# Optimization experiments

Hardware: AMD Instinct MI355X
Metric: run time of the kernel (lower is better)

The kernel has to match this reference:

```python
import jax, jax.numpy as jnp
import numpy as np

NS = 16384   # N*S support examples
NQ = 16384   # N*Q query examples
D = 64       # embedding dim
N_CLASSES = 64


def setup_inputs() -> dict:
    key = jax.random.key(0)
    k1, k2, k3 = jax.random.split(key, 3)
    support_embeddings = jax.random.normal(k1, (NS, D), dtype=jnp.float32)
    query_embeddings = jax.random.normal(k2, (NQ, D), dtype=jnp.float32)
    labels = jax.random.randint(k3, (NS,), 0, N_CLASSES)
    support_labels_onehot = jax.nn.one_hot(labels, N_CLASSES, dtype=jnp.float32)
    return {
        "support_embeddings": support_embeddings,
        "query_embeddings": query_embeddings,
        "support_labels_onehot": support_labels_onehot,
    }


def reference(support_embeddings, query_embeddings, support_labels_onehot):
    # Pairwise L2 distance via ||q||^2 + ||s||^2 - 2 q.s (same math as
    # tf.norm(q[:,None,:] - s[None,:,:], axis=2) without the [NQ,NS,D] blowup).
    sq_s = jnp.sum(support_embeddings * support_embeddings, axis=-1)  # [NS]
    sq_q = jnp.sum(query_embeddings * query_embeddings, axis=-1)      # [NQ]
    cross = jnp.einsum('qd,sd->qs', query_embeddings, support_embeddings)  # [NQ,NS]
    d2 = sq_q[:, None] + sq_s[None, :] - 2.0 * cross
    distance = jnp.sqrt(jnp.maximum(d2, 0.0))
    # top_k(-distance, k=1) == first argmin along support axis
    indices = jnp.argmin(distance, axis=1)                 # [NQ]
    labels_x = jnp.argmax(support_labels_onehot, axis=1)   # [NS]
    labels_pred = labels_x[indices]                        # [NQ] gather
    num_classes = support_labels_onehot.shape[1]
    labels_prob = jax.nn.one_hot(labels_pred, num_classes, dtype=support_labels_onehot.dtype)
    return labels_prob
```

## Files before the change

### kernel.cpp

```cpp
#include <hip/hip_runtime.h>


#define NTOT   16384
#define DIM    64
#define EPS_COEF 0.004f
#define EPS_ABS  0.05f
#define CINIT_COEF (-0.499f)
#define FLT_BIG 3.4e38f

typedef __attribute__((ext_vector_type(8))) short short8;
typedef __attribute__((ext_vector_type(4))) float float4v;

__device__ __forceinline__ ushort f16_bits(float x) {
  union { _Float16 f; ushort u; } c;
  c.f = (_Float16)x;
  return c.u;
}

__device__ __forceinline__ void pin8(short8& v) {
  asm volatile("" : "+v"(v));
}

__global__ __launch_bounds__(256) void k_prep(
    const float* __restrict__ S, const float* __restrict__ Q,
    ushort* __restrict__ Sh, ushort* __restrict__ Qh,
    float* __restrict__ sqS, float* __restrict__ sqQ,
    float* __restrict__ S_T) {
  __shared__ float tile[64][65];
  const int tid = threadIdx.x;
  const bool isS = blockIdx.x < 256;
  const int rbase = (blockIdx.x & 255) * 64;
  const float* __restrict__ src = isS ? S : Q;
  ushort* __restrict__ dh = isS ? Sh : Qh;

  const int tx = tid & 63;
  const int ty = tid >> 6;
#pragma unroll
  for (int i = 0; i < 16; ++i) {
    const int r = i * 4 + ty;
    tile[r][tx] = src[(size_t)(rbase + r) * DIM + tx];
  }
  __syncthreads();

  if (isS) {
#pragma unroll
    for (int i = 0; i < 16; ++i) {
      const int d = i * 4 + ty;
      S_T[(size_t)d * NTOT + rbase + tx] = tile[tx][d];
    }
  }

  const int panel = tid >> 6;
  const int half = (tid >> 5) & 1;
  const int slot0 = (tid & 31) * 2;
#pragma unroll
  for (int ss = 0; ss < 2; ++ss) {
    const int s = slot0 + ss;
    const int m = s & 15;
    const int q8 = s >> 4;
    const int row = panel * 16 + m;
    const int kb = half * 32 + q8 * 8;
    short8 hv;
#pragma unroll
    for (int j = 0; j < 8; ++j) hv[j] = (short)f16_bits(tile[row][kb + j]);
    const size_t goff =
        (size_t)((rbase >> 4) + panel) * 1024 + (size_t)half * 512 + (size_t)s * 8;
    *(short8*)&dh[goff] = hv;
  }

  if (tid < 64) {
    float acc = 0.0f;
#pragma unroll
    for (int d = 0; d < DIM; ++d) {
      const float v = tile[tid][d];
      acc = fmaf(v, v, acc);
    }
    (isS ? sqS : sqQ)[rbase + tid] = acc;
  }
}


#define MFMA16F(A, B, C) __builtin_amdgcn_mfma_f32_16x16x32_f16(A, B, C, 0, 0, 0)

#define STEP_COMPUTE(H0, H1, SQ)                                           \
  do {                                                                     \
    float4v cinit;                                                         \
    cinit[0] = CINIT_COEF * SQ.x;                                          \
    cinit[1] = CINIT_COEF * SQ.y;                                          \
    cinit[2] = CINIT_COEF * SQ.z;                                          \
    cinit[3] = CINIT_COEF * SQ.w;                                          \
    _Pragma("unroll")                                                      \
    for (int t = 0; t < 4; ++t) {                                          \
      float4v a = MFMA16F(H0, qh[t][0], cinit);                            \
      a = MFMA16F(H1, qh[t][1], a);                                        \
      bmr[t] = fmaxf(bmr[t], fmaxf(fmaxf(a[0], a[1]), fmaxf(a[2], a[3]))); \
    }                                                                      \
  } while (0)

template <int BST>
__global__ __launch_bounds__(256, 3) void k_phaseA(
    const ushort* __restrict__ Sh, const ushort* __restrict__ Qh,
    const float* __restrict__ sqS, float* __restrict__ bmin) {
  constexpr int NSB = NTOT / (16 * BST);
  const int tid = threadIdx.x;
  const int l = tid & 63;
  const int w = tid >> 6;
  const int lm = l & 15;
  const int lq = l >> 4;
  const int split = blockIdx.x;
  const int qbase = blockIdx.y * 64;
  const int sbase = split * 2048 + w * 512;

  short8 qh[4][2];
#pragma unroll
  for (int t = 0; t < 4; ++t) {
    const size_t pb = (size_t)((qbase >> 4) + t) * 1024 + (size_t)l * 8;
    qh[t][0] = *(const short8*)&Qh[pb];
    qh[t][1] = *(const short8*)&Qh[pb + 512];
  }
#pragma unroll
  for (int t = 0; t < 4; ++t) {
    pin8(qh[t][0]);
    pin8(qh[t][1]);
  }

  const ushort* pSh = Sh + (size_t)(sbase >> 4) * 1024 + (size_t)l * 8;
  const float* psq = sqS + sbase + lq * 4;

  short8 h0a = *(const short8*)(pSh);
  short8 h1a = *(const short8*)(pSh + 512);
  float4 sqa = *(const float4*)(psq);
  short8 h0b = *(const short8*)(pSh + 1024);
  short8 h1b = *(const short8*)(pSh + 1024 + 512);
  float4 sqb = *(const float4*)(psq + 16);

  float bmr[4] = {-FLT_BIG, -FLT_BIG, -FLT_BIG, -FLT_BIG};

  for (int st = 0; st < 32; st += 2) {
    STEP_COMPUTE(h0a, h1a, sqa);
    if (st + 2 < 32) {
      const int off = (st + 2) * 1024;
      h0a = *(const short8*)(pSh + off);
      h1a = *(const short8*)(pSh + off + 512);
      sqa = *(const float4*)(psq + (st + 2) * 16);
    }
    STEP_COMPUTE(h0b, h1b, sqb);
    if (st + 3 < 32) {
      const int off = (st + 3) * 1024;
      h0b = *(const short8*)(pSh + off);
      h1b = *(const short8*)(pSh + off + 512);
      sqb = *(const float4*)(psq + (st + 3) * 16);
    }
    if (((st + 1) & (BST - 1)) == (BST - 1)) {
      const int gb = split * (128 / BST) + w * (32 / BST) + ((st + 1) / BST);
#pragma unroll
      for (int t = 0; t < 4; ++t) {
        float v = bmr[t];
        v = fmaxf(v, __shfl_xor(v, 16, 64));
        v = fmaxf(v, __shfl_xor(v, 32, 64));
        if (lq == 0) bmin[(size_t)(qbase + t * 16 + lm) * NSB + gb] = -2.0f * v;
        bmr[t] = -FLT_BIG;
      }
    }
  }
}

template <int SBLK>
__global__ __launch_bounds__(256) void k_phaseB(
    const float* __restrict__ S_T,
    const float* __restrict__ Q,
    const float* __restrict__ sqS, const float* __restrict__ sqQ,
    const float* __restrict__ bmin,
    const float* __restrict__ onehot, float* __restrict__ out) {
  constexpr int NSB = NTOT / SBLK;
  constexpr int NB64 = NSB / 64;
  constexpr int SPL = SBLK / 64;

  __shared__ float sQrow[4][64];
  const int lane = threadIdx.x & 63;
  const int w = threadIdx.x >> 6;
  const int q = blockIdx.x * 4 + w;

  if (lane < 16)
    *(float4*)&sQrow[w][lane * 4] = *(const float4*)&Q[(size_t)q * DIM + lane * 4];
  __syncthreads();

  const float eps = EPS_COEF * sqQ[q] + EPS_ABS;

  float bv[NB64];
#pragma unroll
  for (int j = 0; j < NB64; ++j) bv[j] = bmin[(size_t)q * NSB + j * 64 + lane];
  float m = bv[0];
#pragma unroll
  for (int j = 1; j < NB64; ++j) m = fminf(m, bv[j]);
#pragma unroll
  for (int d = 1; d < 64; d <<= 1) m = fminf(m, __shfl_xor(m, d, 64));
  const float thr = m + eps;

  float bk = FLT_BIG;
  int bi = 0;
#pragma unroll
  for (int j = 0; j < NB64; ++j) {
    unsigned long long msk = __ballot(bv[j] <= thr);
    while (msk) {
      const int b = j * 64 + (__ffsll((long long)msk) - 1);
      msk &= msk - 1;
      const int s0 = b * SBLK + lane * SPL;
      if (SPL == 2) {
        float a0 = 0.f, a1 = 0.f;
#pragma unroll
        for (int c = 0; c < 16; ++c) {
          const float4 qv = *(const float4*)&sQrow[w][c * 4];
          const float2 x0 = *(const float2*)&S_T[(size_t)(c * 4 + 0) * NTOT + s0];
          const float2 x1 = *(const float2*)&S_T[(size_t)(c * 4 + 1) * NTOT + s0];
          const float2 x2 = *(const float2*)&S_T[(size_t)(c * 4 + 2) * NTOT + s0];
          const float2 x3 = *(const float2*)&S_T[(size_t)(c * 4 + 3) * NTOT + s0];
          a0 = fmaf(qv.x, x0.x, a0); a1 = fmaf(qv.x, x0.y, a1);
          a0 = fmaf(qv.y, x1.x, a0); a1 = fmaf(qv.y, x1.y, a1);
          a0 = fmaf(qv.z, x2.x, a0); a1 = fmaf(qv.z, x2.y, a1);
          a0 = fmaf(qv.w, x3.x, a0); a1 = fmaf(qv.w, x3.y, a1);
        }
        const float2 sq2 = *(const float2*)&sqS[s0];
        const float k0 = fmaf(-2.f, a0, sq2.x);
        const float k1 = fmaf(-2.f, a1, sq2.y);
        bool u;
        u = k0 < bk; bk = u ? k0 : bk; bi = u ? s0 : bi;
        u = k1 < bk; bk = u ? k1 : bk; bi = u ? (s0 + 1) : bi;
      } else {
        float a0 = 0.f, a1 = 0.f, a2 = 0.f, a3 = 0.f;
#pragma unroll
        for (int c = 0; c < 16; ++c) {
          const float4 qv = *(const float4*)&sQrow[w][c * 4];
          const float4 s0v = *(const float4*)&S_T[(size_t)(c * 4 + 0) * NTOT + s0];
          const float4 s1v = *(const float4*)&S_T[(size_t)(c * 4 + 1) * NTOT + s0];
          const float4 s2v = *(const float4*)&S_T[(size_t)(c * 4 + 2) * NTOT + s0];
          const float4 s3v = *(const float4*)&S_T[(size_t)(c * 4 + 3) * NTOT + s0];
          a0 = fmaf(qv.x, s0v.x, a0); a1 = fmaf(qv.x, s0v.y, a1);
          a2 = fmaf(qv.x, s0v.z, a2); a3 = fmaf(qv.x, s0v.w, a3);
          a0 = fmaf(qv.y, s1v.x, a0); a1 = fmaf(qv.y, s1v.y, a1);
          a2 = fmaf(qv.y, s1v.z, a2); a3 = fmaf(qv.y, s1v.w, a3);
          a0 = fmaf(qv.z, s2v.x, a0); a1 = fmaf(qv.z, s2v.y, a1);
          a2 = fmaf(qv.z, s2v.z, a2); a3 = fmaf(qv.z, s2v.w, a3);
          a0 = fmaf(qv.w, s3v.x, a0); a1 = fmaf(qv.w, s3v.y, a1);
          a2 = fmaf(qv.w, s3v.z, a2); a3 = fmaf(qv.w, s3v.w, a3);
        }
        const float4 sq4 = *(const float4*)&sqS[s0];
        const float k0 = fmaf(-2.f, a0, sq4.x);
        const float k1 = fmaf(-2.f, a1, sq4.y);
        const float k2 = fmaf(-2.f, a2, sq4.z);
        const float k3 = fmaf(-2.f, a3, sq4.w);
        bool u;
        u = k0 < bk; bk = u ? k0 : bk; bi = u ? s0 : bi;
        u = k1 < bk; bk = u ? k1 : bk; bi = u ? (s0 + 1) : bi;
        u = k2 < bk; bk = u ? k2 : bk; bi = u ? (s0 + 2) : bi;
        u = k3 < bk; bk = u ? k3 : bk; bi = u ? (s0 + 3) : bi;
      }
    }
  }
#pragma unroll
  for (int d = 1; d < 64; d <<= 1) {
    const float ok = __shfl_xor(bk, d, 64);
    const int oi = __shfl_xor(bi, d, 64);
    const bool u = (ok < bk) || (ok == bk && oi < bi);
    bk = u ? ok : bk;
    bi = u ? oi : bi;
  }
  const float ov = onehot[(size_t)bi * 64 + lane];
  const unsigned long long lmask = __ballot(ov > 0.5f);
  const int label = __ffsll((long long)lmask) - 1;
  out[(size_t)q * 64 + lane] = (lane == label) ? 1.0f : 0.0f;
}

extern "C" void kernel_launch(void* const* d_in, const int* in_sizes, int n_in,
                              void* d_out, int out_size, void* d_ws, size_t ws_size,
                              hipStream_t stream) {
  const float* S = (const float*)d_in[0];
  const float* Q = (const float*)d_in[1];
  const float* OH = (const float*)d_in[2];
  float* out = (float*)d_out;

  char* ws = (char*)d_ws;
  ushort* Sh = (ushort*)ws;
  ushort* Qh = (ushort*)(ws + (2u << 20));
  float* S_T = (float*)(ws + (4u << 20));
  float* sqS = (float*)(ws + (8u << 20));
  float* sqQ = (float*)(ws + (8u << 20) + (64u << 10));
  float* bmin = (float*)(ws + (8u << 20) + (128u << 10));

  k_prep<<<dim3(512), 256, 0, stream>>>(S, Q, Sh, Qh, sqS, sqQ, S_T);

  if (ws_size >= (17u << 20)) {
    k_phaseA<8><<<dim3(8, NTOT / 64), 256, 0, stream>>>(Sh, Qh, sqS, bmin);
    k_phaseB<128><<<dim3(NTOT / 4), 256, 0, stream>>>(S_T, Q, sqS, sqQ,
                                                      bmin, OH, out);
  } else {
    k_phaseA<16><<<dim3(8, NTOT / 64), 256, 0, stream>>>(Sh, Qh, sqS, bmin);
    k_phaseB<256><<<dim3(NTOT / 4), 256, 0, stream>>>(S_T, Q, sqS, sqQ,
                                                      bmin, OH, out);
  }
  (void)in_sizes; (void)n_in; (void)out_size; (void)ws_size;
}
```

Baseline: 153.3 us.

## Fuse prep and both phases into one cooperative persistent kernel with grid syncs

Merges the three kernel launches into a single cooperative kernel. It loops over virtual blocks for each stage and uses grid-wide syncs between prep, phase A and phase B. The aim is to remove launch overhead and the inter-kernel drain/fill gaps. In exchange, each block runs with fixed occupancy across all phases (launch bounds of 4 blocks per CU instead of 3 for phase A), pays for grid.sync, and issues host-side attribute and occupancy queries on every call.

```diff
diff --git a/kernel.cpp b/kernel.cpp
--- a/kernel.cpp
+++ b/kernel.cpp
@@ -1,4 +1,7 @@
 #include <hip/hip_runtime.h>
+#include <hip/hip_cooperative_groups.h>
+
+namespace cg = cooperative_groups;
 
 
 #define NTOT   16384
@@ -21,15 +24,15 @@
   asm volatile("" : "+v"(v));
 }
 
-__global__ __launch_bounds__(256) void k_prep(
-    const float* __restrict__ S, const float* __restrict__ Q,
+
+__device__ __forceinline__ void prep_body(
+    int vb, const float* __restrict__ S, const float* __restrict__ Q,
     ushort* __restrict__ Sh, ushort* __restrict__ Qh,
     float* __restrict__ sqS, float* __restrict__ sqQ,
-    float* __restrict__ S_T) {
-  __shared__ float tile[64][65];
+    float* __restrict__ S_T, float (*tile)[65]) {
   const int tid = threadIdx.x;
-  const bool isS = blockIdx.x < 256;
-  const int rbase = (blockIdx.x & 255) * 64;
+  const bool isS = vb < 256;
+  const int rbase = (vb & 255) * 64;
   const float* __restrict__ src = isS ? S : Q;
   ushort* __restrict__ dh = isS ? Sh : Qh;
 
@@ -77,8 +80,8 @@
     }
     (isS ? sqS : sqQ)[rbase + tid] = acc;
   }
-}
-
+  __syncthreads();
+}
 
 #define MFMA16F(A, B, C) __builtin_amdgcn_mfma_f32_16x16x32_f16(A, B, C, 0, 0, 0)
 
@@ -98,17 +101,16 @@
   } while (0)
 
 template <int BST>
-__global__ __launch_bounds__(256, 3) void k_phaseA(
-    const ushort* __restrict__ Sh, const ushort* __restrict__ Qh,
-    const float* __restrict__ sqS, float* __restrict__ bmin) {
+__device__ __forceinline__ void phaseA_body(
+    int split, int qbase, const ushort* __restrict__ Sh,
+    const ushort* __restrict__ Qh, const float* __restrict__ sqS,
+    float* __restrict__ bmin) {
   constexpr int NSB = NTOT / (16 * BST);
   const int tid = threadIdx.x;
   const int l = tid & 63;
   const int w = tid >> 6;
   const int lm = l & 15;
   const int lq = l >> 4;
-  const int split = blockIdx.x;
-  const int qbase = blockIdx.y * 64;
   const int sbase = split * 2048 + w * 512;
 
   short8 qh[4][2];
@@ -166,20 +168,18 @@
 }
 
 template <int SBLK>
-__global__ __launch_bounds__(256) void k_phaseB(
-    const float* __restrict__ S_T,
-    const float* __restrict__ Q,
+__device__ __forceinline__ void phaseB_body(
+    int u, const float* __restrict__ S_T, const float* __restrict__ Q,
     const float* __restrict__ sqS, const float* __restrict__ sqQ,
-    const float* __restrict__ bmin,
-    const float* __restrict__ onehot, float* __restrict__ out) {
+    const float* __restrict__ bmin, const float* __restrict__ onehot,
+    float* __restrict__ out, float (*sQrow)[64]) {
   constexpr int NSB = NTOT / SBLK;
   constexpr int NB64 = NSB / 64;
   constexpr int SPL = SBLK / 64;
 
-  __shared__ float sQrow[4][64];
   const int lane = threadIdx.x & 63;
   const int w = threadIdx.x >> 6;
-  const int q = blockIdx.x * 4 + w;
+  const int q = u * 4 + w;
 
   if (lane < 16)
     *(float4*)&sQrow[w][lane * 4] = *(const float4*)&Q[(size_t)q * DIM + lane * 4];
@@ -223,9 +223,9 @@
         const float2 sq2 = *(const float2*)&sqS[s0];
         const float k0 = fmaf(-2.f, a0, sq2.x);
         const float k1 = fmaf(-2.f, a1, sq2.y);
-        bool u;
-        u = k0 < bk; bk = u ? k0 : bk; bi = u ? s0 : bi;
-        u = k1 < bk; bk = u ? k1 : bk; bi = u ? (s0 + 1) : bi;
+        bool uu;
+        uu = k0 < bk; bk = uu ? k0 : bk; bi = uu ? s0 : bi;
+        uu = k1 < bk; bk = uu ? k1 : bk; bi = uu ? (s0 + 1) : bi;
       } else {
         float a0 = 0.f, a1 = 0.f, a2 = 0.f, a3 = 0.f;
 #pragma unroll
@@ -249,11 +249,11 @@
         const float k1 = fmaf(-2.f, a1, sq4.y);
         const float k2 = fmaf(-2.f, a2, sq4.z);
         const float k3 = fmaf(-2.f, a3, sq4.w);
-        bool u;
-        u = k0 < bk; bk = u ? k0 : bk; bi = u ? s0 : bi;
-        u = k1 < bk; bk = u ? k1 : bk; bi = u ? (s0 + 1) : bi;
-        u = k2 < bk; bk = u ? k2 : bk; bi = u ? (s0 + 2) : bi;
-        u = k3 < bk; bk = u ? k3 : bk; bi = u ? (s0 + 3) : bi;
+        bool uu;
+        uu = k0 < bk; bk = uu ? k0 : bk; bi = uu ? s0 : bi;
+        uu = k1 < bk; bk = uu ? k1 : bk; bi = uu ? (s0 + 1) : bi;
+        uu = k2 < bk; bk = uu ? k2 : bk; bi = uu ? (s0 + 2) : bi;
+        uu = k3 < bk; bk = uu ? k3 : bk; bi = uu ? (s0 + 3) : bi;
       }
     }
   }
@@ -261,14 +261,64 @@
   for (int d = 1; d < 64; d <<= 1) {
     const float ok = __shfl_xor(bk, d, 64);
     const int oi = __shfl_xor(bi, d, 64);
-    const bool u = (ok < bk) || (ok == bk && oi < bi);
-    bk = u ? ok : bk;
-    bi = u ? oi : bi;
+    const bool uu = (ok < bk) || (ok == bk && oi < bi);
+    bk = uu ? ok : bk;
+    bi = uu ? oi : bi;
   }
   const float ov = onehot[(size_t)bi * 64 + lane];
   const unsigned long long lmask = __ballot(ov > 0.5f);
   const int label = __ffsll((long long)lmask) - 1;
   out[(size_t)q * 64 + lane] = (lane == label) ? 1.0f : 0.0f;
+  __syncthreads();
+}
+
+__global__ __launch_bounds__(256, 4) void k_mega(
+    const float* __restrict__ S, const float* __restrict__ Q,
+    const float* __restrict__ OH, float* __restrict__ out,
+    ushort* __restrict__ Sh, ushort* __restrict__ Qh,
+    float* __restrict__ sqS, float* __restrict__ sqQ,
+    float* __restrict__ S_T, float* __restrict__ bmin) {
+  __shared__ float tile[64][65];
+  __shared__ float sQrow[4][64];
+  cg::grid_group grid = cg::this_grid();
+  const int nb = gridDim.x;
+
+  for (int u = blockIdx.x; u < 512; u += nb)
+    prep_body(u, S, Q, Sh, Qh, sqS, sqQ, S_T, tile);
+  grid.sync();
+
+  for (int u = blockIdx.x; u < 2048; u += nb)
+    phaseA_body<8>(u & 7, (u >> 3) * 64, Sh, Qh, sqS, bmin);
+  grid.sync();
+
+  for (int u = blockIdx.x; u < 4096; u += nb)
+    phaseB_body<128>(u, S_T, Q, sqS, sqQ, bmin, OH, out, sQrow);
+}
+
+__global__ __launch_bounds__(256) void k_prep_fb(
+    const float* __restrict__ S, const float* __restrict__ Q,
+    ushort* __restrict__ Sh, ushort* __restrict__ Qh,
+    float* __restrict__ sqS, float* __restrict__ sqQ,
+    float* __restrict__ S_T) {
+  __shared__ float tile[64][65];
+  prep_body(blockIdx.x, S, Q, Sh, Qh, sqS, sqQ, S_T, tile);
+}
+
+template <int BST>
+__global__ __launch_bounds__(256, 3) void k_phaseA_fb(
+    const ushort* __restrict__ Sh, const ushort* __restrict__ Qh,
+    const float* __restrict__ sqS, float* __restrict__ bmin) {
+  phaseA_body<BST>(blockIdx.x, blockIdx.y * 64, Sh, Qh, sqS, bmin);
+}
+
+template <int SBLK>
+__global__ __launch_bounds__(256) void k_phaseB_fb(
+    const float* __restrict__ S_T, const float* __restrict__ Q,
+    const float* __restrict__ sqS, const float* __restrict__ sqQ,
+    const float* __restrict__ bmin, const float* __restrict__ onehot,
+    float* __restrict__ out) {
+  __shared__ float sQrow[4][64];
+  phaseB_body<SBLK>(blockIdx.x, S_T, Q, sqS, sqQ, bmin, onehot, out, sQrow);
 }
 
 extern "C" void kernel_launch(void* const* d_in, const int* in_sizes, int n_in,
@@ -287,16 +337,42 @@
   float* sqQ = (float*)(ws + (8u << 20) + (64u << 10));
   float* bmin = (float*)(ws + (8u << 20) + (128u << 10));
 
-  k_prep<<<dim3(512), 256, 0, stream>>>(S, Q, Sh, Qh, sqS, sqQ, S_T);
-
-  if (ws_size >= (17u << 20)) {
-    k_phaseA<8><<<dim3(8, NTOT / 64), 256, 0, stream>>>(Sh, Qh, sqS, bmin);
-    k_phaseB<128><<<dim3(NTOT / 4), 256, 0, stream>>>(S_T, Q, sqS, sqQ,
-                                                      bmin, OH, out);
+  const bool bigWs = ws_size >= (17u << 20);
+
+  bool useCoop = false;
+  int gridBlocks = 0;
+  if (bigWs) {
+    int dev = 0, coopAttr = 0, maxB = 0;
+    if (hipGetDevice(&dev) == hipSuccess &&
+        hipDeviceGetAttribute(&coopAttr, hipDeviceAttributeCooperativeLaunch,
+                              dev) == hipSuccess &&
+        coopAttr != 0 &&
+        hipOccupancyMaxActiveBlocksPerMultiprocessor(
+            &maxB, (const void*)k_mega, 256, 0) == hipSuccess &&
+        maxB >= 1) {
+      gridBlocks = maxB * 256;
+      if (gridBlocks > 1024) gridBlocks = 1024;
+      useCoop = true;
+    }
+  }
+
+  if (useCoop) {
+    const float* a0 = S; const float* a1 = Q; const float* a2 = OH;
+    float* a3 = out; ushort* a4 = Sh; ushort* a5 = Qh;
+    float* a6 = sqS; float* a7 = sqQ; float* a8 = S_T; float* a9 = bmin;
+    void* args[] = {&a0, &a1, &a2, &a3, &a4, &a5, &a6, &a7, &a8, &a9};
+    hipLaunchCooperativeKernel((void*)k_mega, dim3(gridBlocks), dim3(256),
+                               args, 0, stream);
+  } else if (bigWs) {
+    k_prep_fb<<<dim3(512), 256, 0, stream>>>(S, Q, Sh, Qh, sqS, sqQ, S_T);
+    k_phaseA_fb<8><<<dim3(8, NTOT / 64), 256, 0, stream>>>(Sh, Qh, sqS, bmin);
+    k_phaseB_fb<128><<<dim3(NTOT / 4), 256, 0, stream>>>(S_T, Q, sqS, sqQ,
+                                                         bmin, OH, out);
   } else {
-    k_phaseA<16><<<dim3(8, NTOT / 64), 256, 0, stream>>>(Sh, Qh, sqS, bmin);
-    k_phaseB<256><<<dim3(NTOT / 4), 256, 0, stream>>>(S_T, Q, sqS, sqQ,
-                                                      bmin, OH, out);
+    k_prep_fb<<<dim3(512), 256, 0, stream>>>(S, Q, Sh, Qh, sqS, sqQ, S_T);
+    k_phaseA_fb<16><<<dim3(8, NTOT / 64), 256, 0, stream>>>(Sh, Qh, sqS, bmin);
+    k_phaseB_fb<256><<<dim3(NTOT / 4), 256, 0, stream>>>(S_T, Q, sqS, sqQ,
+                                                         bmin, OH, out);
   }
   (void)in_sizes; (void)n_in; (void)out_size; (void)ws_size;
 }
```

After: 323.9 us. 111% more time.
